# Optimization experiments

Hardware: AMD Instinct MI355X
Metric: run time of the kernel (lower is better)

Reference implementation:

```python
import jax, jax.numpy as jnp
import numpy as np

KS = 4                                  # kernel_size per axis
K = KS ** 3                             # 64 spatial filter bins
RADIUS = np.float32(1.5 * 6 * 0.025 / 2.0)   # filter_extent / 2 = 0.1125
N_REAL = 20000                          # fluid particles (index N_REAL = far dummy)
E_PAD = 1200000                         # padded edge count


def ball_to_cube(u):
    # volume-preserving unit-ball -> [-1,1]^3 cube map (Griepentrog et al., as in
    # Open3D-ML 'ball_to_cube_volume_preserving'): ball -> cylinder -> cube.
    eps = 1e-9
    x, y, z = u[..., 0], u[..., 1], u[..., 2]
    sq = x * x + y * y + z * z
    norm = jnp.sqrt(sq + eps)
    rxy2 = x * x + y * y
    polar = 1.25 * z * z > rxy2          # top/bottom cone region
    s = jnp.where(polar,
                  jnp.sqrt(3.0 * norm / (norm + jnp.abs(z) + eps)),
                  norm / jnp.sqrt(rxy2 + eps))
    xc = x * s
    yc = y * s
    zc = jnp.where(polar, jnp.sign(z) * norm, 1.5 * z)
    degen = sq < 1e-12
    xc = jnp.where(degen, 0.0, xc)
    yc = jnp.where(degen, 0.0, yc)
    zc = jnp.where(degen, 0.0, zc)
    # cylinder -> cube: inverse concentric (Shirley-Chiu) area-preserving map on xy
    r = jnp.sqrt(xc * xc + yc * yc + eps)
    c1 = jnp.abs(xc) >= jnp.abs(yc)
    xs = jnp.where(jnp.abs(xc) < eps, eps, xc)
    ys = jnp.where(jnp.abs(yc) < eps, eps, yc)
    fop = np.float32(4.0 / np.pi)
    a = jnp.where(c1, jnp.sign(xc) * r, jnp.sign(yc) * r * fop * jnp.arctan(xc / ys))
    b = jnp.where(c1, jnp.sign(xc) * r * fop * jnp.arctan(yc / xs), jnp.sign(yc) * r)
    tiny = (xc * xc + yc * yc) < 1e-12
    a = jnp.where(tiny, 0.0, a)
    b = jnp.where(tiny, 0.0, b)
    return jnp.stack([a, b, zc], axis=-1)


def cconv(feat, pos, src, dst, W, b):
    # ContinuousConv: normalize=False, align_corners=True, linear interpolation,
    # poly6 window on r^2/radius^2, self-neighbors excluded in the edge list.
    offs = (pos[dst] - pos[src]) / RADIUS              # (E,3), inside unit ball
    r2 = jnp.sum(offs * offs, axis=-1)
    win = jnp.clip((1.0 - r2) ** 3, 0.0, 1.0)          # window_poly6; 0 on pad edges
    g = jnp.clip((ball_to_cube(offs) * 0.5 + 0.5) * (KS - 1), 0.0, KS - 1)
    f0f = jnp.floor(g)
    t = g - f0f                                         # trilinear fractions
    f0 = f0f.astype(jnp.int32)
    fj = feat[dst] * win[:, None]                       # (E,Cin) windowed neighbor feats
    n = pos.shape[0]
    cin = feat.shape[1]
    B = jnp.zeros((n * K, cin), feat.dtype)             # per-query per-bin accumulator
    for c in range(8):                                  # 8 trilinear corners
        w = jnp.ones_like(r2)
        kf = jnp.zeros_like(src)
        for ax in range(3):
            bit = (c >> (2 - ax)) & 1
            ia = jnp.minimum(f0[:, ax] + bit, KS - 1)
            w = w * (t[:, ax] if bit else 1.0 - t[:, ax])
            kf = kf * KS + ia
        B = B + jax.ops.segment_sum(fj * w[:, None], src * K + kf, num_segments=n * K)
    out = jnp.einsum('nki,kio->no', B.reshape(n, K, cin), W.reshape(K, cin, -1))
    return out + b


def forward(pos, feats, edge_src, edge_dst, conv0_w, conv0_b, dense0_w, dense0_b,
            conv1_w, conv1_b, dense1_w, dense1_b, conv2_w, conv2_b, dense2_w, dense2_b,
            conv3_w, conv3_b, dense3_w, dense3_b):
    f = jnp.concatenate([jnp.ones_like(pos[:, :1]), feats], axis=-1)   # 13 channels
    x = jnp.concatenate([cconv(f, pos, edge_src, edge_dst, conv0_w, conv0_b),
                         f @ dense0_w + dense0_b], axis=-1)            # 64 + 32 = 96
    layers = [(conv1_w, conv1_b, dense1_w, dense1_b),
              (conv2_w, conv2_b, dense2_w, dense2_b),
              (conv3_w, conv3_b, dense3_w, dense3_b)]
    for cw, cb, dw, db in layers:
        inp = jax.nn.relu(x)
        y = cconv(inp, pos, edge_src, edge_dst, cw, cb) + inp @ dw + db
        x = (y + x) if y.shape[-1] == x.shape[-1] else y               # residual 64->64
    return (x * (1.0 / 128.0))[:N_REAL]                                # pos_correction


def setup_inputs() -> dict:
    rng = np.random.default_rng(0)
    spacing = 0.05                                  # 2 * particle_radius
    g = np.arange(28)
    pts = np.stack(np.meshgrid(g, g, g, indexing='ij'), -1).reshape(-1, 3).astype(np.float64) * spacing
    pts = pts[:N_REAL] + rng.uniform(-0.012, 0.012, (N_REAL, 3))
    # fixed-radius neighbor search, excluding self (radius_search_ignore_query_points)
    r2 = float(RADIUS) ** 2
    sq = (pts ** 2).sum(-1)
    src_l, dst_l = [], []
    for s in range(0, N_REAL, 1000):
        q = pts[s:s + 1000]
        d2 = (q ** 2).sum(-1)[:, None] + sq[None, :] - 2.0 * (q @ pts.T)
        ii, jj = np.nonzero(d2 < r2)
        ii = ii + s
        keep = ii != jj
        src_l.append(ii[keep])
        dst_l.append(jj[keep])
    src = np.concatenate(src_l).astype(np.int32)[:E_PAD]
    dst = np.concatenate(dst_l).astype(np.int32)[:E_PAD]
    pad = E_PAD - src.size
    src = np.concatenate([src, np.zeros(pad, np.int32)])
    dst = np.concatenate([dst, np.full(pad, N_REAL, np.int32)])   # edges to far dummy -> window 0
    pos = np.concatenate([pts, [[1e3, 1e3, 1e3]]], 0).astype(np.float32)
    key = jax.random.key(0)
    ks = jax.random.split(key, 12)
    def w(k, shape, fan_in):
        return jax.random.normal(k, shape, jnp.float32) * np.float32(1.0 / np.sqrt(fan_in))
    return {
        'pos': jnp.asarray(pos),
        'feats': jax.random.normal(ks[0], (N_REAL + 1, 12), jnp.float32),
        'edge_src': jnp.asarray(src),
        'edge_dst': jnp.asarray(dst),
        'conv0_w': w(ks[1], (KS, KS, KS, 13, 64), 13 * 27),
        'conv0_b': jnp.zeros((64,), jnp.float32),
        'dense0_w': w(ks[2], (13, 32), 13),
        'dense0_b': jnp.zeros((32,), jnp.float32),
        'conv1_w': w(ks[3], (KS, KS, KS, 96, 64), 96 * 27),
        'conv1_b': jnp.zeros((64,), jnp.float32),
        'dense1_w': w(ks[4], (96, 64), 96),
        'dense1_b': jnp.zeros((64,), jnp.float32),
        'conv2_w': w(ks[5], (KS, KS, KS, 64, 64), 64 * 27),
        'conv2_b': jnp.zeros((64,), jnp.float32),
        'dense2_w': w(ks[6], (64, 64), 64),
        'dense2_b': jnp.zeros((64,), jnp.float32),
        'conv3_w': w(ks[7], (KS, KS, KS, 64, 3), 64 * 27),
        'conv3_b': jnp.zeros((3,), jnp.float32),
        'dense3_w': w(ks[8], (64, 3), 64),
        'dense3_b': jnp.zeros((3,), jnp.float32),
    }


def reference(pos, feats, edge_src, edge_dst, conv0_w, conv0_b, dense0_w, dense0_b,
              conv1_w, conv1_b, dense1_w, dense1_b, conv2_w, conv2_b, dense2_w, dense2_b,
              conv3_w, conv3_b, dense3_w, dense3_b):
    return forward(pos, feats, edge_src, edge_dst, conv0_w, conv0_b, dense0_w, dense0_b,
                   conv1_w, conv1_b, dense1_w, dense1_b, conv2_w, conv2_b, dense2_w, dense2_b,
                   conv3_w, conv3_b, dense3_w, dense3_b)
```

## Files before the change

### kernel.cpp

```cpp
#include <hip/hip_runtime.h>
#include <math.h>

#define NPTS   20001
#define NREAL  20000
#define EPAD   1200000
#define KK     64
#define RADF   0.1125f

typedef _Float16 half8_t __attribute__((ext_vector_type(8)));
typedef float    floatx4 __attribute__((ext_vector_type(4)));

__device__ __forceinline__ float sgnf(float v){ return v>0.f ? 1.f : (v<0.f ? -1.f : 0.f); }

__global__ void k_find_ereal(const int* __restrict__ dst, int* __restrict__ ereal){
  int lo=0, hi=EPAD;
  while(lo<hi){ int mid=(lo+hi)>>1; if(dst[mid]==NREAL) hi=mid; else lo=mid+1; }
  *ereal = lo;
}

__global__ void k_csr(const int* __restrict__ src, const int* __restrict__ erealp,
                      int* __restrict__ row_start){
  int i = blockIdx.x*blockDim.x + threadIdx.x;
  if(i > NPTS) return;
  int E = *erealp;
  int lo=0, hi=E;
  while(lo<hi){ int mid=(lo+hi)>>1; if(src[mid] < i) lo=mid+1; else hi=mid; }
  row_start[i] = lo;
}

__global__ void k_build_f(const float* __restrict__ feats, float* __restrict__ f){
  int idx = blockIdx.x*blockDim.x + threadIdx.x;
  if(idx >= NPTS*13) return;
  int i = idx/13, c = idx - i*13;
  f[idx] = (c==0) ? 1.f : feats[i*12 + (c-1)];
}

__device__ __forceinline__ void edge_geom(float ox, float oy, float oz,
                                          float& win, float& t0, float& t1, float& t2, int& f0p){
  const float eps = 1e-9f;
  float sq = ox*ox + oy*oy + oz*oz;
  float u = 1.f - sq;
  win = fminf(fmaxf(u*u*u, 0.f), 1.f);
  float norm = sqrtf(sq + eps);
  float rxy2 = ox*ox + oy*oy;
  bool polar = (1.25f*oz*oz > rxy2);
  float s_p = sqrtf(3.f*norm/(norm + fabsf(oz) + eps));
  float s_n = norm / sqrtf(rxy2 + eps);
  float s = polar ? s_p : s_n;
  float xc = ox*s, yc = oy*s;
  float zc = polar ? sgnf(oz)*norm : 1.5f*oz;
  if(sq < 1e-12f){ xc = 0.f; yc = 0.f; zc = 0.f; }
  float r = sqrtf(xc*xc + yc*yc + eps);
  bool c1 = fabsf(xc) >= fabsf(yc);
  float xs = (fabsf(xc) < eps) ? eps : xc;
  float ys = (fabsf(yc) < eps) ? eps : yc;
  const float fop = 1.2732395447351628f;
  float a = c1 ? sgnf(xc)*r : sgnf(yc)*r*fop*atanf(xc/ys);
  float b = c1 ? sgnf(xc)*r*fop*atanf(yc/xs) : sgnf(yc)*r;
  if(xc*xc + yc*yc < 1e-12f){ a = 0.f; b = 0.f; }
  float g0 = fminf(fmaxf((a *0.5f+0.5f)*3.f, 0.f), 3.f);
  float g1 = fminf(fmaxf((b *0.5f+0.5f)*3.f, 0.f), 3.f);
  float g2 = fminf(fmaxf((zc*0.5f+0.5f)*3.f, 0.f), 3.f);
  float f00 = floorf(g0), f01 = floorf(g1), f02 = floorf(g2);
  t0 = g0 - f00; t1 = g1 - f01; t2 = g2 - f02;
  f0p = (int)f00 | ((int)f01 << 2) | ((int)f02 << 4);
}

__global__ __launch_bounds__(256) void k_geom(const float* __restrict__ pos,
    const int* __restrict__ esrc, const int* __restrict__ edst,
    float4* __restrict__ gw, int4* __restrict__ gmz)
{
  int e = blockIdx.x*blockDim.x + threadIdx.x;
  if(e >= EPAD) return;
  const int sn = esrc[e], d = edst[e];
  const float ox = (pos[d*3+0]-pos[sn*3+0])/RADF;
  const float oy = (pos[d*3+1]-pos[sn*3+1])/RADF;
  const float oz = (pos[d*3+2]-pos[sn*3+2])/RADF;
  float win, t0, t1, t2; int f0p;
  edge_geom(ox, oy, oz, win, t0, t1, t2, f0p);
  const int i0 = f0p & 3, i1 = (f0p>>2) & 3, i2 = f0p >> 4;
  const int X0 = i0 << 4, X1 = ((i0+1)&3) << 4;
  const int Y0 = i1 << 2, Y1 = ((i1+1)&3) << 2;
  const int Z0 = i2, Z1 = (i2+1) & 3;
  const float wx0 = win*(1.f-t0), wx1 = win*t0;
  const float wy0 = 1.f-t1, wy1 = t1;
  const float wz0 = 1.f-t2, wz1 = t2;
  gw[e] = make_float4(wx0*wy0, wx0*wy1, wx1*wy0, wx1*wy1);
  const int p0 = Z0 & 1;
  const float zA = p0 ? wz1 : wz0;
  const int   cA = p0 ? Z1 : Z0;
  const int   cB = p0 ? Z0 : Z1;
  const int cells0 = (X0|Y0|cA) | ((X0|Y1|cA)<<8) | ((X1|Y0|cA)<<16) | ((X1|Y1|cA)<<24);
  const int cells1 = (X0|Y0|cB) | ((X0|Y1|cB)<<8) | ((X1|Y0|cB)<<16) | ((X1|Y1|cB)<<24);
  gmz[e] = make_int4(__float_as_int(zA), cells0, cells1, d);
}

template<int RELU, int OUT3>
__global__ __launch_bounds__(256) void k_scat64m(
    const float* __restrict__ feat, const float4* __restrict__ gw,
    const int4* __restrict__ gmz, const int* __restrict__ row_start,
    float* __restrict__ B, int node_base,
    const float* __restrict__ W3, float* __restrict__ out)
{
  __shared__ __align__(16) _Float16 Wh[64][40];
  __shared__ __align__(16) _Float16 Wl[64][40];
  __shared__ __align__(16) _Float16 Fh[64][40];
  __shared__ __align__(16) _Float16 Fl[64][40];
  __shared__ __align__(16) float4 Sq[32];
  __shared__ __align__(16) int4   Smd[32];
  __shared__ float red[16];

  const int tid  = threadIdx.x;
  const int node = node_base + blockIdx.x;
  const int wv   = tid >> 6;
  const int lane = tid & 63;
  const int frow = lane & 15, fk = (lane >> 4) * 8;

  floatx4 acc[4];
  #pragma unroll
  for(int nt=0;nt<4;++nt){ acc[nt][0]=0.f; acc[nt][1]=0.f; acc[nt][2]=0.f; acc[nt][3]=0.f; }

  half8_t hz;
  #pragma unroll
  for(int q8=0;q8<8;++q8) hz[q8] = (_Float16)0;

  const int e0 = row_start[node], e1 = row_start[node+1];

  for(int eb = e0; eb < e1; eb += 32){
    const int n = (e1 - eb < 32) ? (e1 - eb) : 32;
    __syncthreads();
    if(wv == 0){
      if(lane < 32){
        int ei = eb + lane; if(ei >= e1) ei = e1 - 1;
        Sq[lane]  = gw[ei];
        Smd[lane] = gmz[ei];
      }
    } else {
      for(int j = tid - 64; j < 640; j += 192){
        if(j < 320) ((half8_t*)Wh)[j]       = hz;
        else        ((half8_t*)Wl)[j - 320] = hz;
      }
    }
    __syncthreads();
    {
      half8_t hreg, lreg;
      #pragma unroll
      for(int j=0;j<8;++j){
        const int dst = Smd[wv*8 + j].w;
        float v = feat[(size_t)dst*64 + lane];
        if(RELU) v = fmaxf(v, 0.f);
        _Float16 h = (_Float16)v;
        hreg[j] = h;
        lreg[j] = (_Float16)(v - (float)h);
      }
      *(half8_t*)&Fh[lane][wv*8] = hreg;
      *(half8_t*)&Fl[lane][wv*8] = lreg;
    }
    if(lane < 8){
      const int ei = wv*8 + lane;
      if(ei < n){
        const float4 q  = Sq[ei];
        const int4   md = Smd[ei];
        const float zA = __int_as_float(md.x), zB = 1.f - zA;
        #pragma unroll
        for(int t=0;t<8;++t){
          const int   cells = (t < 4) ? md.y : md.z;
          const float zz    = (t < 4) ? zA : zB;
          const int   cell  = (cells >> ((t & 3) * 8)) & 255;
          const float qq    = ((t&3)==0) ? q.x : ((t&3)==1) ? q.y : ((t&3)==2) ? q.z : q.w;
          const float wgt   = qq * zz;
          const _Float16 h  = (_Float16)wgt;
          Wh[cell][ei] = h;
          Wl[cell][ei] = (_Float16)(wgt - (float)h);
        }
      }
    }
    __syncthreads();
    const half8_t ah = *(const half8_t*)&Wh[wv*16 + frow][fk];
    const half8_t al = *(const half8_t*)&Wl[wv*16 + frow][fk];
    #pragma unroll
    for(int nt=0; nt<4; ++nt){
      const half8_t bh = *(const half8_t*)&Fh[nt*16 + frow][fk];
      const half8_t bl = *(const half8_t*)&Fl[nt*16 + frow][fk];
      acc[nt] = __builtin_amdgcn_mfma_f32_16x16x32_f16(ah, bh, acc[nt], 0, 0, 0);
      acc[nt] = __builtin_amdgcn_mfma_f32_16x16x32_f16(al, bh, acc[nt], 0, 0, 0);
      acc[nt] = __builtin_amdgcn_mfma_f32_16x16x32_f16(ah, bl, acc[nt], 0, 0, 0);
    }
  }

  if(!OUT3){
    float* Bg = B + (size_t)blockIdx.x*4096;
    #pragma unroll
    for(int nt=0;nt<4;++nt)
      #pragma unroll
      for(int r=0;r<4;++r){
        const int cell = wv*16 + (lane>>4)*4 + r;
        Bg[cell*64 + nt*16 + (lane&15)] = acc[nt][r];
      }
  } else {
    float s0=0.f, s1=0.f, s2=0.f;
    #pragma unroll
    for(int nt=0;nt<4;++nt){
      #pragma unroll
      for(int r=0;r<4;++r){
        const int cell = wv*16 + (lane>>4)*4 + r;
        const int j3   = (cell*64 + nt*16 + (lane&15)) * 3;
        const float v  = acc[nt][r];
        s0 = fmaf(v, W3[j3+0], s0);
        s1 = fmaf(v, W3[j3+1], s1);
        s2 = fmaf(v, W3[j3+2], s2);
      }
    }
    #pragma unroll
    for(int off = 32; off > 0; off >>= 1){
      s0 += __shfl_down(s0, off);
      s1 += __shfl_down(s1, off);
      s2 += __shfl_down(s2, off);
    }
    if(lane == 0){
      red[wv*4+0] = s0; red[wv*4+1] = s1; red[wv*4+2] = s2;
    }
    __syncthreads();
    if(tid == 0 && node < NREAL){
      out[node*3+0] += (red[0]+red[4]+red[8] +red[12])*(1.f/128.f);
      out[node*3+1] += (red[1]+red[5]+red[9] +red[13])*(1.f/128.f);
      out[node*3+2] += (red[2]+red[6]+red[10]+red[14])*(1.f/128.f);
    }
  }
}

template<int RELU>
__global__ __launch_bounds__(128) void k_scat96(
    const float* __restrict__ feat, const float4* __restrict__ gw,
    const int4* __restrict__ gmz, const int* __restrict__ row_start,
    float* __restrict__ B, int node_base)
{
  constexpr int CIN = 96, BSZ = KK*CIN, NP = 48;
  __shared__ __align__(16) float Bl[BSZ];
  __shared__ __align__(16) float4 Sgw[64];
  __shared__ __align__(16) int4   Smd[64];
  const int tid  = threadIdx.x;
  const int node = node_base + blockIdx.x;

  for(int j = tid*4; j < BSZ; j += 512)
    *(float4*)&Bl[j] = make_float4(0.f,0.f,0.f,0.f);

  const int e0 = row_start[node], e1 = row_start[node+1];
  const int wv   = tid >> 6;
  const int lane = tid & 63;
  const bool act = (lane < NP);
  float2* Bp2 = (float2*)Bl;

  for(int eb = e0; eb < e1; eb += 64){
    const int n = (e1 - eb < 64) ? (e1 - eb) : 64;
    __syncthreads();
    if(lane < n){
      if(wv == 0) Sgw[lane] = gw[eb + lane];
      else        Smd[lane] = gmz[eb + lane];
    }
    __syncthreads();
    if(act){
      #pragma unroll 2
      for(int i = 0; i < n; ++i){
        const float4 q  = Sgw[i];
        const int4   md = Smd[i];
        const float zA = __int_as_float(md.x);
        const float z  = wv ? (1.f - zA) : zA;
        const int   cp = wv ? md.z : md.y;
        float2 v2 = ((const float2*)(feat + (size_t)md.w*CIN))[lane];
        if(RELU){ v2.x = fmaxf(v2.x,0.f); v2.y = fmaxf(v2.y,0.f); }
        v2.x *= z; v2.y *= z;
        const int b0 = ( cp        & 255)*NP + lane;
        const int b1 = ((cp >> 8)  & 255)*NP + lane;
        const int b2 = ((cp >> 16) & 255)*NP + lane;
        const int b3 = (((unsigned)cp) >> 24)*NP + lane;
        float2 o0 = Bp2[b0], o1 = Bp2[b1], o2 = Bp2[b2], o3 = Bp2[b3];
        o0.x = fmaf(q.x, v2.x, o0.x); o0.y = fmaf(q.x, v2.y, o0.y);
        o1.x = fmaf(q.y, v2.x, o1.x); o1.y = fmaf(q.y, v2.y, o1.y);
        o2.x = fmaf(q.z, v2.x, o2.x); o2.y = fmaf(q.z, v2.y, o2.y);
        o3.x = fmaf(q.w, v2.x, o3.x); o3.y = fmaf(q.w, v2.y, o3.y);
        Bp2[b0] = o0; Bp2[b1] = o1; Bp2[b2] = o2; Bp2[b3] = o3;
      }
    }
  }
  __syncthreads();

  float* Bg = B + (size_t)blockIdx.x*BSZ;
  for(int j = tid*4; j < BSZ; j += 512)
    *(float4*)&Bg[j] = *(const float4*)&Bl[j];
}

__global__ __launch_bounds__(128) void k_scat13(
    const float* __restrict__ feat, const float4* __restrict__ gw,
    const int4* __restrict__ gmz, const int* __restrict__ row_start,
    float* __restrict__ B, int node_base)
{
  constexpr int CIN = 13, BSZ = KK*CIN, ESW = 4, CSTRIDE = BSZ + 8;
  __shared__ __align__(16) float Bl[ESW*CSTRIDE];
  const int tid  = threadIdx.x;
  const int node = node_base + blockIdx.x;

  for(int j = tid; j < ESW*CSTRIDE; j += 128) Bl[j] = 0.f;

  const int e0 = row_start[node], e1 = row_start[node+1];
  const int wv   = tid >> 6;
  const int lane = tid & 63;
  const int slot = lane >> 4;
  const int c    = lane & 15;
  const bool act = (c < CIN);
  float* Bp = Bl + slot*CSTRIDE;
  __syncthreads();

  if(act){
    for(int e = e0 + slot; e < e1; e += ESW){
      const float4 q  = gw[e];
      const int4   md = gmz[e];
      const float zA = __int_as_float(md.x);
      const float z  = wv ? (1.f - zA) : zA;
      const int   cp = wv ? md.z : md.y;
      float v = feat[(size_t)md.w*CIN + c] * z;
      const int b0 = ( cp        & 255)*CIN + c;
      const int b1 = ((cp >> 8)  & 255)*CIN + c;
      const int b2 = ((cp >> 16) & 255)*CIN + c;
      const int b3 = (((unsigned)cp) >> 24)*CIN + c;
      float o0 = Bp[b0], o1 = Bp[b1], o2 = Bp[b2], o3 = Bp[b3];
      o0 = fmaf(q.x, v, o0); o1 = fmaf(q.y, v, o1);
      o2 = fmaf(q.z, v, o2); o3 = fmaf(q.w, v, o3);
      Bp[b0] = o0; Bp[b1] = o1; Bp[b2] = o2; Bp[b3] = o3;
    }
  }
  __syncthreads();

  float* Bg = B + (size_t)blockIdx.x*BSZ;
  for(int j = tid*4; j < BSZ; j += 512){
    float4 a = *(const float4*)&Bl[j];
    #pragma unroll
    for(int k = 1; k < ESW; ++k){
      const float4 t = *(const float4*)&Bl[k*CSTRIDE + j];
      a.x += t.x; a.y += t.y; a.z += t.z; a.w += t.w;
    }
    *(float4*)&Bg[j] = a;
  }
}

__global__ void k_cvtW(const float* __restrict__ W, _Float16* __restrict__ WhT,
                       _Float16* __restrict__ WlT, int Kd)
{
  int idx = blockIdx.x*blockDim.x + threadIdx.x;
  if(idx >= 64*Kd) return;
  int o = idx / Kd, k = idx - o*Kd;
  float w = W[(size_t)k*64 + o];
  _Float16 h = (_Float16)w;
  WhT[idx] = h;
  WlT[idx] = (_Float16)(w - (float)h);
}

__global__ __launch_bounds__(256) void k_gemm_mfma(
    const float* __restrict__ A, const _Float16* __restrict__ WhT,
    const _Float16* __restrict__ WlT, float* __restrict__ P,
    int M, int Kd, int node_base, int ksteps_per)
{
  __shared__ __align__(16) _Float16 Ah[64][40];
  __shared__ __align__(16) _Float16 Al[64][40];
  __shared__ __align__(16) _Float16 Bh[64][40];
  __shared__ __align__(16) _Float16 Blo[64][40];
  const int tid = threadIdx.x;
  const int mbase = blockIdx.x * 64;
  const int s = blockIdx.y;
  const int kt0 = s * ksteps_per * 32;
  const int kt1 = min(Kd, kt0 + ksteps_per*32);
  const int wv = tid >> 6, lane = tid & 63;
  const int row  = tid >> 2;
  const int kseg = (tid & 3) * 8;
  const int frow = lane & 15, fk = (lane >> 4) * 8;

  floatx4 acc[4];
  #pragma unroll
  for(int c=0;c<4;++c){ acc[c][0]=0.f; acc[c][1]=0.f; acc[c][2]=0.f; acc[c][3]=0.f; }

  const int grow = mbase + row;
  const float* Arow = (grow < M) ? (A + (size_t)grow*Kd) : nullptr;
  const _Float16* WhRow = WhT + (size_t)row*Kd;
  const _Float16* WlRow = WlT + (size_t)row*Kd;

  for(int kt = kt0; kt < kt1; kt += 32){
    float av[8];
    if(Arow){
      *(float4*)&av[0] = *(const float4*)(Arow + kt + kseg);
      *(float4*)&av[4] = *(const float4*)(Arow + kt + kseg + 4);
    } else {
      #pragma unroll
      for(int j=0;j<8;++j) av[j] = 0.f;
    }
    half8_t hv, lv;
    #pragma unroll
    for(int j=0;j<8;++j){
      _Float16 h = (_Float16)av[j];
      hv[j] = h;
      lv[j] = (_Float16)(av[j] - (float)h);
    }
    half8_t wh = *(const half8_t*)(WhRow + kt + kseg);
    half8_t wl = *(const half8_t*)(WlRow + kt + kseg);
    __syncthreads();
    *(half8_t*)&Ah[row][kseg]  = hv;
    *(half8_t*)&Al[row][kseg]  = lv;
    *(half8_t*)&Bh[row][kseg]  = wh;
    *(half8_t*)&Blo[row][kseg] = wl;
    __syncthreads();
    const half8_t ah = *(const half8_t*)&Ah[wv*16 + frow][fk];
    const half8_t al = *(const half8_t*)&Al[wv*16 + frow][fk];
    #pragma unroll
    for(int c=0;c<4;++c){
      const half8_t bh = *(const half8_t*)&Bh[c*16 + frow][fk];
      const half8_t bl = *(const half8_t*)&Blo[c*16 + frow][fk];
      acc[c] = __builtin_amdgcn_mfma_f32_16x16x32_f16(ah, bh, acc[c], 0, 0, 0);
      acc[c] = __builtin_amdgcn_mfma_f32_16x16x32_f16(al, bh, acc[c], 0, 0, 0);
      acc[c] = __builtin_amdgcn_mfma_f32_16x16x32_f16(ah, bl, acc[c], 0, 0, 0);
    }
  }

  const int prow0 = mbase + wv*16 + (lane>>4)*4;
  const int pcol  = lane & 15;
  #pragma unroll
  for(int c=0;c<4;++c){
    #pragma unroll
    for(int r=0;r<4;++r){
      const int rr = prow0 + r;
      if(rr < M)
        P[((size_t)s*NPTS + node_base + rr)*64 + c*16 + pcol] = acc[c][r];
    }
  }
}

template<int S>
__global__ void k_combine(const float* __restrict__ P, float* __restrict__ x,
                          int ldout, int colofs)
{
  int idx = blockIdx.x*blockDim.x + threadIdx.x;
  if(idx >= NPTS*16) return;
  int node = idx >> 4, c4 = (idx & 15) * 4;
  float4 s = *(const float4*)(P + (size_t)node*64 + c4);
  #pragma unroll
  for(int k=1;k<S;++k){
    float4 t = *(const float4*)(P + ((size_t)k*NPTS + node)*64 + c4);
    s.x+=t.x; s.y+=t.y; s.z+=t.z; s.w+=t.w;
  }
  float* xp = x + (size_t)node*ldout + colofs + c4;
  float4 o = *(float4*)xp;
  o.x+=s.x; o.y+=s.y; o.z+=s.z; o.w+=s.w;
  *(float4*)xp = o;
}

__global__ void k_dense0(const float* __restrict__ f, const float* __restrict__ dW,
                         const float* __restrict__ db, const float* __restrict__ cb0,
                         float* __restrict__ out)
{
  int idx = blockIdx.x*blockDim.x + threadIdx.x;
  if(idx >= NPTS*96) return;
  int i = idx/96, c = idx - i*96;
  if(c < 64){ out[idx] = cb0[c]; return; }
  int o = c - 64;
  float s = db[o];
  const float* row = f + (size_t)i*13;
  #pragma unroll
  for(int j=0;j<13;++j) s = fmaf(row[j], dW[j*32+o], s);
  out[idx] = s;
}

__global__ void k_dense(const float* __restrict__ in, int cin,
                        const float* __restrict__ dW, const float* __restrict__ db,
                        const float* __restrict__ cb, const float* __restrict__ resid,
                        float* __restrict__ out)
{
  int idx = blockIdx.x*blockDim.x + threadIdx.x;
  if(idx >= NPTS*64) return;
  int i = idx >> 6, o = idx & 63;
  float s = db[o] + cb[o];
  if(resid) s += resid[idx];
  const float* row = in + (size_t)i*cin;
  for(int c=0;c<cin;++c) s = fmaf(fmaxf(row[c],0.f), dW[c*64+o], s);
  out[idx] = s;
}

__global__ void k_dense3(const float* __restrict__ x2, const float* __restrict__ dW,
                         const float* __restrict__ db, const float* __restrict__ cb,
                         float* __restrict__ out)
{
  int idx = blockIdx.x*blockDim.x + threadIdx.x;
  if(idx >= NREAL*3) return;
  int i = idx/3, o = idx - i*3;
  float s = db[o] + cb[o];
  const float* row = x2 + (size_t)i*64;
  for(int c=0;c<64;++c) s = fmaf(fmaxf(row[c],0.f), dW[c*3+o], s);
  out[idx] = s * (1.f/128.f);
}

static inline size_t alup(size_t x){ return (x + 255) & ~(size_t)255; }

static inline int calc_rows(size_t bcap, int cin, int want){
  size_t perrow = (size_t)KK * cin * 4;
  size_t r = (perrow > 0) ? bcap / perrow : 0;
  if(r >= (size_t)want) return want;
  r = (r / 128) * 128;
  if(r < 128) r = 128;
  return (int)r;
}

extern "C" void kernel_launch(void* const* d_in, const int* in_sizes, int n_in,
                              void* d_out, int out_size, void* d_ws, size_t ws_size,
                              hipStream_t stream)
{
  const float* pos   = (const float*)d_in[0];
  const float* feats = (const float*)d_in[1];
  const int*   esrc  = (const int*)d_in[2];
  const int*   edst  = (const int*)d_in[3];
  const float* c0w = (const float*)d_in[4];
  const float* c0b = (const float*)d_in[5];
  const float* d0w = (const float*)d_in[6];
  const float* d0b = (const float*)d_in[7];
  const float* c1w = (const float*)d_in[8];
  const float* c1b = (const float*)d_in[9];
  const float* d1w = (const float*)d_in[10];
  const float* d1b = (const float*)d_in[11];
  const float* c2w = (const float*)d_in[12];
  const float* c2b = (const float*)d_in[13];
  const float* d2w = (const float*)d_in[14];
  const float* d2b = (const float*)d_in[15];
  const float* c3w = (const float*)d_in[16];
  const float* c3b = (const float*)d_in[17];
  const float* d3w = (const float*)d_in[18];
  const float* d3b = (const float*)d_in[19];
  float* out = (float*)d_out;

  char* w = (char*)d_ws;
  size_t off = 0;
  float* f  = (float*)(w+off); off += alup((size_t)NPTS*13*4);
  float* x0 = (float*)(w+off); off += alup((size_t)NPTS*96*4);
  float* x1 = (float*)(w+off); off += alup((size_t)NPTS*64*4);
  float* x2 = (float*)(w+off); off += alup((size_t)NPTS*64*4);
  int* row_start = (int*)(w+off); off += alup((size_t)(NPTS+1)*4);
  int* ereal = (int*)(w+off);     off += alup(16);
  float4* gw = (float4*)(w+off);  off += alup((size_t)EPAD*16);
  int4*  gmz = (int4*)(w+off);    off += alup((size_t)EPAD*16);
  float* P  = (float*)(w+off); off += alup((size_t)8*NPTS*64*4);
  _Float16* whT = (_Float16*)(w+off); off += alup((size_t)64*6144*2);
  _Float16* wlT = (_Float16*)(w+off); off += alup((size_t)64*6144*2);
  float* B = (float*)(w+off);
  size_t bcap = (ws_size > off) ? (ws_size - off) : 0;

  k_find_ereal<<<1,1,0,stream>>>(edst, ereal);
  k_csr<<<(NPTS+1+255)/256,256,0,stream>>>(esrc, ereal, row_start);
  k_build_f<<<(NPTS*13+255)/256,256,0,stream>>>(feats, f);
  k_geom<<<(EPAD+255)/256,256,0,stream>>>(pos, esrc, edst, gw, gmz);

  k_dense0<<<(NPTS*96+255)/256,256,0,stream>>>(f, d0w, d0b, c0b, x0);
  {
    k_cvtW<<<(64*832+255)/256,256,0,stream>>>(c0w, whT, wlT, 832);
    int rows = calc_rows(bcap, 13, 8192);
    for(int base = 0; base < NPTS; base += rows){
      int m = (NPTS - base < rows) ? (NPTS - base) : rows;
      k_scat13<<<m,128,0,stream>>>(f, gw, gmz, row_start, B, base);
      k_gemm_mfma<<<dim3((m+63)/64, 8),256,0,stream>>>(B, whT, wlT, P, m, 832, base, 4);
    }
    k_combine<8><<<(NPTS*16+255)/256,256,0,stream>>>(P, x0, 96, 0);
  }

  k_dense<<<(NPTS*64+255)/256,256,0,stream>>>(x0, 96, d1w, d1b, c1b, nullptr, x1);
  {
    k_cvtW<<<(64*6144+255)/256,256,0,stream>>>(c1w, whT, wlT, 6144);
    int rows = calc_rows(bcap, 96, 4096);
    for(int base = 0; base < NPTS; base += rows){
      int m = (NPTS - base < rows) ? (NPTS - base) : rows;
      k_scat96<1><<<m,128,0,stream>>>(x0, gw, gmz, row_start, B, base);
      k_gemm_mfma<<<dim3((m+63)/64, 8),256,0,stream>>>(B, whT, wlT, P, m, 6144, base, 24);
    }
    k_combine<8><<<(NPTS*16+255)/256,256,0,stream>>>(P, x1, 64, 0);
  }

  k_dense<<<(NPTS*64+255)/256,256,0,stream>>>(x1, 64, d2w, d2b, c2b, x1, x2);
  {
    k_cvtW<<<(64*4096+255)/256,256,0,stream>>>(c2w, whT, wlT, 4096);
    int rows = calc_rows(bcap, 64, 4096);
    for(int base = 0; base < NPTS; base += rows){
      int m = (NPTS - base < rows) ? (NPTS - base) : rows;
      k_scat64m<1,0><<<m,256,0,stream>>>(x1, gw, gmz, row_start, B, base, nullptr, nullptr);
      k_gemm_mfma<<<dim3((m+63)/64, 8),256,0,stream>>>(B, whT, wlT, P, m, 4096, base, 16);
    }
    k_combine<8><<<(NPTS*16+255)/256,256,0,stream>>>(P, x2, 64, 0);
  }

  k_dense3<<<(NREAL*3+255)/256,256,0,stream>>>(x2, d3w, d3b, c3b, out);
  k_scat64m<1,1><<<NPTS,256,0,stream>>>(x2, gw, gmz, row_start, nullptr, 0, c3w, out);
}
```

Baseline: 988.9 us.

## Use MFMA scatter for 96-channel conv and pre-split features to fp16 pairs

Replaces the LDS atomic-free scalar scatter for the 96-channel layer with an MFMA-based kernel that builds a sparse weight matrix per edge chunk and multiplies it against gathered features using split-fp16 (hi/lo) products. Adds a pre-pass that applies ReLU once and packs each feature into an fp16 hi/lo pair, so the scatter kernels gather one 32-bit word per element instead of converting per edge. This removes redundant per-edge conversion and the serial FMA loop into shared memory. In exchange it adds extra conversion passes and workspace, and the 3-term split-fp16 product loses a little precision compared with fp32.

```diff
diff --git a/kernel.cpp b/kernel.cpp
--- a/kernel.cpp
+++ b/kernel.cpp
@@ -11,6 +11,8 @@
 typedef float    floatx4 __attribute__((ext_vector_type(4)));
 
 __device__ __forceinline__ float sgnf(float v){ return v>0.f ? 1.f : (v<0.f ? -1.f : 0.f); }
+__device__ __forceinline__ _Float16 lo16(unsigned u){ return __builtin_bit_cast(_Float16, (unsigned short)(u & 0xffffu)); }
+__device__ __forceinline__ _Float16 hi16(unsigned u){ return __builtin_bit_cast(_Float16, (unsigned short)(u >> 16)); }
 
 __global__ void k_find_ereal(const int* __restrict__ dst, int* __restrict__ ereal){
   int lo=0, hi=EPAD;
@@ -33,6 +35,16 @@
   if(idx >= NPTS*13) return;
   int i = idx/13, c = idx - i*13;
   f[idx] = (c==0) ? 1.f : feats[i*12 + (c-1)];
+}
+
+__global__ void k_cvtF(const float* __restrict__ x, unsigned* __restrict__ Fp, int total){
+  int idx = blockIdx.x*blockDim.x + threadIdx.x;
+  if(idx >= total) return;
+  float v = fmaxf(x[idx], 0.f);
+  _Float16 h = (_Float16)v;
+  _Float16 l = (_Float16)(v - (float)h);
+  Fp[idx] = (unsigned)__builtin_bit_cast(unsigned short, h)
+          | ((unsigned)__builtin_bit_cast(unsigned short, l) << 16);
 }
 
 __device__ __forceinline__ void edge_geom(float ox, float oy, float oz,
@@ -95,9 +107,9 @@
   gmz[e] = make_int4(__float_as_int(zA), cells0, cells1, d);
 }
 
-template<int RELU, int OUT3>
+template<int OUT3>
 __global__ __launch_bounds__(256) void k_scat64m(
-    const float* __restrict__ feat, const float4* __restrict__ gw,
+    const unsigned* __restrict__ Fp, const float4* __restrict__ gw,
     const int4* __restrict__ gmz, const int* __restrict__ row_start,
     float* __restrict__ B, int node_base,
     const float* __restrict__ W3, float* __restrict__ out)
@@ -147,11 +159,9 @@
       #pragma unroll
       for(int j=0;j<8;++j){
         const int dst = Smd[wv*8 + j].w;
-        float v = feat[(size_t)dst*64 + lane];
-        if(RELU) v = fmaxf(v, 0.f);
-        _Float16 h = (_Float16)v;
-        hreg[j] = h;
-        lreg[j] = (_Float16)(v - (float)h);
+        const unsigned u = Fp[(size_t)dst*64 + lane];
+        hreg[j] = lo16(u);
+        lreg[j] = hi16(u);
       }
       *(half8_t*)&Fh[lane][wv*8] = hreg;
       *(half8_t*)&Fl[lane][wv*8] = lreg;
@@ -229,65 +239,111 @@
   }
 }
 
-template<int RELU>
-__global__ __launch_bounds__(128) void k_scat96(
-    const float* __restrict__ feat, const float4* __restrict__ gw,
+__global__ __launch_bounds__(256) void k_scat96m(
+    const unsigned* __restrict__ Fp, const float4* __restrict__ gw,
     const int4* __restrict__ gmz, const int* __restrict__ row_start,
     float* __restrict__ B, int node_base)
 {
-  constexpr int CIN = 96, BSZ = KK*CIN, NP = 48;
-  __shared__ __align__(16) float Bl[BSZ];
-  __shared__ __align__(16) float4 Sgw[64];
-  __shared__ __align__(16) int4   Smd[64];
+  __shared__ __align__(16) _Float16 Wh[64][40];
+  __shared__ __align__(16) _Float16 Wl[64][40];
+  __shared__ __align__(16) _Float16 Fh[96][40];
+  __shared__ __align__(16) _Float16 Fl[96][40];
+  __shared__ __align__(16) float4 Sq[32];
+  __shared__ __align__(16) int4   Smd[32];
+
   const int tid  = threadIdx.x;
   const int node = node_base + blockIdx.x;
-
-  for(int j = tid*4; j < BSZ; j += 512)
-    *(float4*)&Bl[j] = make_float4(0.f,0.f,0.f,0.f);
-
-  const int e0 = row_start[node], e1 = row_start[node+1];
   const int wv   = tid >> 6;
   const int lane = tid & 63;
-  const bool act = (lane < NP);
-  float2* Bp2 = (float2*)Bl;
-
-  for(int eb = e0; eb < e1; eb += 64){
-    const int n = (e1 - eb < 64) ? (e1 - eb) : 64;
-    __syncthreads();
-    if(lane < n){
-      if(wv == 0) Sgw[lane] = gw[eb + lane];
-      else        Smd[lane] = gmz[eb + lane];
-    }
-    __syncthreads();
-    if(act){
-      #pragma unroll 2
-      for(int i = 0; i < n; ++i){
-        const float4 q  = Sgw[i];
-        const int4   md = Smd[i];
-        const float zA = __int_as_float(md.x);
-        const float z  = wv ? (1.f - zA) : zA;
-        const int   cp = wv ? md.z : md.y;
-        float2 v2 = ((const float2*)(feat + (size_t)md.w*CIN))[lane];
-        if(RELU){ v2.x = fmaxf(v2.x,0.f); v2.y = fmaxf(v2.y,0.f); }
-        v2.x *= z; v2.y *= z;
-        const int b0 = ( cp        & 255)*NP + lane;
-        const int b1 = ((cp >> 8)  & 255)*NP + lane;
-        const int b2 = ((cp >> 16) & 255)*NP + lane;
-        const int b3 = (((unsigned)cp) >> 24)*NP + lane;
-        float2 o0 = Bp2[b0], o1 = Bp2[b1], o2 = Bp2[b2], o3 = Bp2[b3];
-        o0.x = fmaf(q.x, v2.x, o0.x); o0.y = fmaf(q.x, v2.y, o0.y);
-        o1.x = fmaf(q.y, v2.x, o1.x); o1.y = fmaf(q.y, v2.y, o1.y);
-        o2.x = fmaf(q.z, v2.x, o2.x); o2.y = fmaf(q.z, v2.y, o2.y);
-        o3.x = fmaf(q.w, v2.x, o3.x); o3.y = fmaf(q.w, v2.y, o3.y);
-        Bp2[b0] = o0; Bp2[b1] = o1; Bp2[b2] = o2; Bp2[b3] = o3;
-      }
-    }
-  }
-  __syncthreads();
-
-  float* Bg = B + (size_t)blockIdx.x*BSZ;
-  for(int j = tid*4; j < BSZ; j += 512)
-    *(float4*)&Bg[j] = *(const float4*)&Bl[j];
+  const int frow = lane & 15, fk = (lane >> 4) * 8;
+
+  floatx4 acc[6];
+  #pragma unroll
+  for(int nt=0;nt<6;++nt){ acc[nt][0]=0.f; acc[nt][1]=0.f; acc[nt][2]=0.f; acc[nt][3]=0.f; }
+
+  half8_t hz;
+  #pragma unroll
+  for(int q8=0;q8<8;++q8) hz[q8] = (_Float16)0;
+
+  const int e0 = row_start[node], e1 = row_start[node+1];
+
+  for(int eb = e0; eb < e1; eb += 32){
+    const int n = (e1 - eb < 32) ? (e1 - eb) : 32;
+    __syncthreads();
+    if(wv == 0){
+      if(lane < 32){
+        int ei = eb + lane; if(ei >= e1) ei = e1 - 1;
+        Sq[lane]  = gw[ei];
+        Smd[lane] = gmz[ei];
+      }
+    } else {
+      for(int j = tid - 64; j < 640; j += 192){
+        if(j < 320) ((half8_t*)Wh)[j]       = hz;
+        else        ((half8_t*)Wl)[j - 320] = hz;
+      }
+    }
+    __syncthreads();
+    {
+      half8_t h0, l0, h1, l1;
+      #pragma unroll
+      for(int j=0;j<8;++j){
+        const int dst = Smd[wv*8 + j].w;
+        const unsigned u = Fp[(size_t)dst*96 + lane];
+        h0[j] = lo16(u);
+        l0[j] = hi16(u);
+        if(lane < 32){
+          const unsigned u2 = Fp[(size_t)dst*96 + 64 + lane];
+          h1[j] = lo16(u2);
+          l1[j] = hi16(u2);
+        }
+      }
+      *(half8_t*)&Fh[lane][wv*8] = h0;
+      *(half8_t*)&Fl[lane][wv*8] = l0;
+      if(lane < 32){
+        *(half8_t*)&Fh[64 + lane][wv*8] = h1;
+        *(half8_t*)&Fl[64 + lane][wv*8] = l1;
+      }
+    }
+    if(lane < 8){
+      const int ei = wv*8 + lane;
+      if(ei < n){
+        const float4 q  = Sq[ei];
+        const int4   md = Smd[ei];
+        const float zA = __int_as_float(md.x), zB = 1.f - zA;
+        #pragma unroll
+        for(int t=0;t<8;++t){
+          const int   cells = (t < 4) ? md.y : md.z;
+          const float zz    = (t < 4) ? zA : zB;
+          const int   cell  = (cells >> ((t & 3) * 8)) & 255;
+          const float qq    = ((t&3)==0) ? q.x : ((t&3)==1) ? q.y : ((t&3)==2) ? q.z : q.w;
+          const float wgt   = qq * zz;
+          const _Float16 h  = (_Float16)wgt;
+          Wh[cell][ei] = h;
+          Wl[cell][ei] = (_Float16)(wgt - (float)h);
+        }
+      }
+    }
+    __syncthreads();
+    const half8_t ah = *(const half8_t*)&Wh[wv*16 + frow][fk];
+    const half8_t al = *(const half8_t*)&Wl[wv*16 + frow][fk];
+    #pragma unroll
+    for(int nt=0; nt<6; ++nt){
+      const half8_t bh = *(const half8_t*)&Fh[nt*16 + frow][fk];
+      const half8_t bl = *(const half8_t*)&Fl[nt*16 + frow][fk];
+      acc[nt] = __builtin_amdgcn_mfma_f32_16x16x32_f16(ah, bh, acc[nt], 0, 0, 0);
+      acc[nt] = __builtin_amdgcn_mfma_f32_16x16x32_f16(al, bh, acc[nt], 0, 0, 0);
+      acc[nt] = __builtin_amdgcn_mfma_f32_16x16x32_f16(ah, bl, acc[nt], 0, 0, 0);
+    }
+  }
+
+  float* Bg = B + (size_t)blockIdx.x*6144;
+  #pragma unroll
+  for(int nt=0;nt<6;++nt)
+    #pragma unroll
+    for(int r=0;r<4;++r){
+      const int cell = wv*16 + (lane>>4)*4 + r;
+      Bg[cell*96 + nt*16 + (lane&15)] = acc[nt][r];
+    }
 }
 
 __global__ __launch_bounds__(128) void k_scat13(
@@ -545,6 +601,8 @@
   float* P  = (float*)(w+off); off += alup((size_t)8*NPTS*64*4);
   _Float16* whT = (_Float16*)(w+off); off += alup((size_t)64*6144*2);
   _Float16* wlT = (_Float16*)(w+off); off += alup((size_t)64*6144*2);
+  unsigned* Fp0 = (unsigned*)(w+off); off += alup((size_t)NPTS*96*4);
+  unsigned* Fp1 = (unsigned*)(w+off); off += alup((size_t)NPTS*64*4);
   float* B = (float*)(w+off);
   size_t bcap = (ws_size > off) ? (ws_size - off) : 0;
 
@@ -560,7 +618,7 @@
     for(int base = 0; base < NPTS; base += rows){
       int m = (NPTS - base < rows) ? (NPTS - base) : rows;
       k_scat13<<<m,128,0,stream>>>(f, gw, gmz, row_start, B, base);
-      k_gemm_mfma<<<dim3((m+63)/64, 8),256,0,stream>>>(B, whT, wlT, P, m, 832, base, 4);
+      k_gemm_mfma<<<dim3((m+63)/64, 8),256,0,stream>>>(B, c0w ? whT : whT, wlT, P, m, 832, base, 4);
     }
     k_combine<8><<<(NPTS*16+255)/256,256,0,stream>>>(P, x0, 96, 0);
   }
@@ -568,10 +626,11 @@
   k_dense<<<(NPTS*64+255)/256,256,0,stream>>>(x0, 96, d1w, d1b, c1b, nullptr, x1);
   {
     k_cvtW<<<(64*6144+255)/256,256,0,stream>>>(c1w, whT, wlT, 6144);
+    k_cvtF<<<(NPTS*96+255)/256,256,0,stream>>>(x0, Fp0, NPTS*96);
     int rows = calc_rows(bcap, 96, 4096);
     for(int base = 0; base < NPTS; base += rows){
       int m = (NPTS - base < rows) ? (NPTS - base) : rows;
-      k_scat96<1><<<m,128,0,stream>>>(x0, gw, gmz, row_start, B, base);
+      k_scat96m<<<m,256,0,stream>>>(Fp0, gw, gmz, row_start, B, base);
       k_gemm_mfma<<<dim3((m+63)/64, 8),256,0,stream>>>(B, whT, wlT, P, m, 6144, base, 24);
     }
     k_combine<8><<<(NPTS*16+255)/256,256,0,stream>>>(P, x1, 64, 0);
@@ -580,15 +639,17 @@
   k_dense<<<(NPTS*64+255)/256,256,0,stream>>>(x1, 64, d2w, d2b, c2b, x1, x2);
   {
     k_cvtW<<<(64*4096+255)/256,256,0,stream>>>(c2w, whT, wlT, 4096);
+    k_cvtF<<<(NPTS*64+255)/256,256,0,stream>>>(x1, Fp1, NPTS*64);
     int rows = calc_rows(bcap, 64, 4096);
     for(int base = 0; base < NPTS; base += rows){
       int m = (NPTS - base < rows) ? (NPTS - base) : rows;
-      k_scat64m<1,0><<<m,256,0,stream>>>(x1, gw, gmz, row_start, B, base, nullptr, nullptr);
+      k_scat64m<0><<<m,256,0,stream>>>(Fp1, gw, gmz, row_start, B, base, nullptr, nullptr);
       k_gemm_mfma<<<dim3((m+63)/64, 8),256,0,stream>>>(B, whT, wlT, P, m, 4096, base, 16);
     }
     k_combine<8><<<(NPTS*16+255)/256,256,0,stream>>>(P, x2, 64, 0);
   }
 
   k_dense3<<<(NREAL*3+255)/256,256,0,stream>>>(x2, d3w, d3b, c3b, out);
-  k_scat64m<1,1><<<NPTS,256,0,stream>>>(x2, gw, gmz, row_start, nullptr, 0, c3w, out);
-}
+  k_cvtF<<<(NPTS*64+255)/256,256,0,stream>>>(x2, Fp1, NPTS*64);
+  k_scat64m<1><<<NPTS,256,0,stream>>>(Fp1, gw, gmz, row_start, nullptr, 0, c3w, out);
+}
```

Measured after the change: 990.5 us. No clear change (+0.2%).
